# Optimization experiments

Hardware: AMD Instinct MI355X
Metric: run time of the kernel (lower is better)

The kernel has to match this reference:

```python
import jax, jax.numpy as jnp
import numpy as np

B, T, H = 256, 2048, 128
LSTM_IN = [24, 128, 128]


def _xavier(key, fan_out, fan_in):
    std = (2.0 / (fan_in + fan_out)) ** 0.5
    return jax.random.normal(key, (fan_out, fan_in), jnp.float32) * std


def setup_inputs() -> dict:
    key = jax.random.key(0)
    ks = jax.random.split(key, 32)
    inp = {}
    inp['scent'] = jax.random.normal(ks[0], (B, T, 3), jnp.float32)
    # fc1: Linear(3,12) + ReLU + Linear(12,24) + ReLU, xavier weights, zero bias
    inp['W1'] = _xavier(ks[1], 12, 3); inp['b1'] = jnp.zeros((12,), jnp.float32)
    inp['W2'] = _xavier(ks[2], 24, 12); inp['b2'] = jnp.zeros((24,), jnp.float32)
    # 3-layer LSTM, PyTorch default init: uniform(-1/sqrt(H), 1/sqrt(H)) for all params
    k = 1.0 / np.sqrt(H)
    for l in range(3):
        d = LSTM_IN[l]
        inp[f'Wih{l}'] = jax.random.uniform(ks[4 + 4 * l], (4 * H, d), jnp.float32, -k, k)
        inp[f'Whh{l}'] = jax.random.uniform(ks[5 + 4 * l], (4 * H, H), jnp.float32, -k, k)
        inp[f'bih{l}'] = jax.random.uniform(ks[6 + 4 * l], (4 * H,), jnp.float32, -k, k)
        inp[f'bhh{l}'] = jax.random.uniform(ks[7 + 4 * l], (4 * H,), jnp.float32, -k, k)
    # fc2: Linear(128,64) + ReLU + Linear(64,32) + ReLU
    inp['Wf1'] = _xavier(ks[20], 64, 128); inp['bf1'] = jnp.zeros((64,), jnp.float32)
    inp['Wf2'] = _xavier(ks[21], 32, 64); inp['bf2'] = jnp.zeros((32,), jnp.float32)
    return inp


def _lstm_layer(x, Wih, Whh, bih, bhh):
    # x: [T, B, D] -> ys: [T, B, H]; PyTorch gate order i, f, g, o
    gx = jnp.einsum('tbd,gd->tbg', x, Wih) + bih + bhh  # [T, B, 4H]

    def step(carry, g_t):
        h, c = carry
        gates = g_t + h @ Whh.T
        i, f, g, o = jnp.split(gates, 4, axis=-1)
        c = jax.nn.sigmoid(f) * c + jax.nn.sigmoid(i) * jnp.tanh(g)
        h = jax.nn.sigmoid(o) * jnp.tanh(c)
        return (h, c), h

    h0 = jnp.zeros((x.shape[1], H), x.dtype)
    (hT, cT), ys = jax.lax.scan(step, (h0, h0), gx)
    return ys, hT, cT


def reference(scent, W1, b1, W2, b2,
              Wih0, Whh0, bih0, bhh0,
              Wih1, Whh1, bih1, bhh1,
              Wih2, Whh2, bih2, bhh2,
              Wf1, bf1, Wf2, bf2):
    # fc1 (pointwise over B*T)
    x = jax.nn.relu(scent @ W1.T + b1)
    x = jax.nn.relu(x @ W2.T + b2)          # [B, T, 24]
    x = jnp.transpose(x, (1, 0, 2))          # [T, B, 24] seq-first
    hs, cs = [], []
    for Wih, Whh, bih, bhh in ((Wih0, Whh0, bih0, bhh0),
                               (Wih1, Whh1, bih1, bhh1),
                               (Wih2, Whh2, bih2, bhh2)):
        x, hT, cT = _lstm_layer(x, Wih, Whh, bih, bhh)
        hs.append(hT); cs.append(cT)
    h = jnp.stack(hs)                        # [3, B, H]
    c = jnp.stack(cs)                        # [3, B, H]
    y = jnp.transpose(x, (1, 0, 2))          # [B, T, H]
    y = jax.nn.relu(y @ Wf1.T + bf1)
    out = jax.nn.relu(y @ Wf2.T + bf2)       # [B, T, 32]
    return out, h, c
```

## Files before the change

kernel.cpp:

```cpp
#include <hip/hip_runtime.h>

#define B 256
#define T 2048
#define HDIM 128
#define CH 256
#define NCHUNK (T / CH)

typedef _Float16 f16;
typedef _Float16 h2 __attribute__((ext_vector_type(2)));
typedef _Float16 f16x8 __attribute__((ext_vector_type(8)));
typedef float f32x4 __attribute__((ext_vector_type(4)));

__device__ __forceinline__ float dot2(h2 a, h2 b, float c) {
#if __has_builtin(__builtin_amdgcn_fdot2)
    return __builtin_amdgcn_fdot2(a, b, c, false);
#else
    return c + (float)a[0] * (float)b[0] + (float)a[1] * (float)b[1];
#endif
}

__device__ __forceinline__ float rcp_(float x) {
#if __has_builtin(__builtin_amdgcn_rcpf)
    return __builtin_amdgcn_rcpf(x);
#else
    return 1.0f / x;
#endif
}
__device__ __forceinline__ float sigm(float x) { return rcp_(1.0f + __expf(-x)); }
__device__ __forceinline__ float tanh_(float x) {
    float e = __expf(-2.0f * fabsf(x));
    float t = fmaf(2.0f, rcp_(1.0f + e), -1.0f);
    return copysignf(t, x);
}

__device__ __forceinline__ void bar() {
    asm volatile("s_waitcnt lgkmcnt(0)" ::: "memory");
    __builtin_amdgcn_s_barrier();
}

__global__ __launch_bounds__(256) void fc1_kernel(
    const float* __restrict__ scent,
    const float* __restrict__ W1, const float* __restrict__ b1,
    const float* __restrict__ W2, const float* __restrict__ b2,
    f16* __restrict__ x1) {
    int r = blockIdx.x * 256 + threadIdx.x;
    int b = r >> 11, t = r & 2047;
    float s0 = scent[r * 3], s1 = scent[r * 3 + 1], s2 = scent[r * 3 + 2];
    float a[12];
#pragma unroll
    for (int i = 0; i < 12; i++) {
        float v = W1[i * 3] * s0 + W1[i * 3 + 1] * s1 + W1[i * 3 + 2] * s2 + b1[i];
        a[i] = fmaxf(v, 0.f);
    }
    union { f16 o[32]; uint4 u[4]; } U;
#pragma unroll
    for (int j = 0; j < 24; j++) {
        float v = b2[j];
#pragma unroll
        for (int i = 0; i < 12; i++) v = fmaf(W2[j * 12 + i], a[i], v);
        U.o[j] = (f16)fmaxf(v, 0.f);
    }
#pragma unroll
    for (int j = 24; j < 32; j++) U.o[j] = (f16)0.f;
    uint4* d4 = (uint4*)(x1 + ((size_t)t * B + b) * 32);
#pragma unroll
    for (int i = 0; i < 4; i++) d4[i] = U.u[i];
}

__global__ __launch_bounds__(256) void pack_kernel(const float* __restrict__ w,
                                                   unsigned int* __restrict__ o) {
    int i = blockIdx.x * 256 + threadIdx.x;
    if (i < 4096) {
        union { h2 h; unsigned int u; } U;
        U.h[0] = (f16)w[2 * i];
        U.h[1] = (f16)w[2 * i + 1];
        o[i] = U.u;
    }
}

template <int KIN, int KREAL, int SP>
__global__ __launch_bounds__(256) void gx_gemm(
    const f16* __restrict__ x,
    const float* __restrict__ Wih,
    const float* __restrict__ bih, const float* __restrict__ bhh,
    f16* __restrict__ gx,
    int t0) {
    constexpr int KF = KIN / 32;
    __shared__ __align__(16) f16 Alds[64 * SP];
    const int tid = threadIdx.x;
    const int mb = blockIdx.x, nb = blockIdx.y;
    const int l = tid & 63, wv = tid >> 6;
    const int lc = l & 15, lg = l >> 4;

    const f16* xrow = x + ((size_t)t0 * B + (size_t)mb * 64) * KIN;
    if (KIN == 128) {
#pragma unroll
        for (int it = 0; it < 4; it++) {
            int row = it * 16 + (tid >> 4), cc = tid & 15;
            uint4 v = *(const uint4*)(xrow + (size_t)row * KIN + cc * 8);
            *(uint4*)(&Alds[row * SP + cc * 8]) = v;
        }
    } else {
        int row = tid >> 2, cc = tid & 3;
        uint4 v = *(const uint4*)(xrow + (size_t)row * KIN + cc * 8);
        *(uint4*)(&Alds[row * SP + cc * 8]) = v;
    }

    const int gbase = nb * 128 + (wv & 1) * 64;
    const int rbase = (wv >> 1) * 32;
    f16x8 bf[4][KF];
    float bias4[4];
#pragma unroll
    for (int gt = 0; gt < 4; gt++) {
        int g = gbase + gt * 16 + lc;
        bias4[gt] = bih[g] + bhh[g];
#pragma unroll
        for (int kf = 0; kf < KF; kf++) {
            f16x8 v;
#pragma unroll
            for (int j = 0; j < 8; j++) {
                int k = kf * 32 + lg * 8 + j;
                v[j] = (k < KREAL) ? (f16)Wih[(size_t)g * KREAL + k] : (f16)0.f;
            }
            bf[gt][kf] = v;
        }
    }
    __syncthreads();

    f32x4 acc[2][4] = {};
#pragma unroll
    for (int kf = 0; kf < KF; kf++) {
#pragma unroll
        for (int rt = 0; rt < 2; rt++) {
            f16x8 af = *(const f16x8*)(&Alds[(rbase + rt * 16 + lc) * SP + kf * 32 + lg * 8]);
#pragma unroll
            for (int gt = 0; gt < 4; gt++)
                acc[rt][gt] = __builtin_amdgcn_mfma_f32_16x16x32_f16(af, bf[gt][kf], acc[rt][gt], 0, 0, 0);
        }
    }
#pragma unroll
    for (int rt = 0; rt < 2; rt++)
#pragma unroll
        for (int gt = 0; gt < 4; gt++)
#pragma unroll
            for (int q = 0; q < 4; q++) {
                int rr = mb * 64 + rbase + rt * 16 + lg * 4 + q;
                int gg = gbase + gt * 16 + lc;
                gx[(size_t)rr * 512 + gg] = (f16)(acc[rt][gt][q] + bias4[gt]);
            }
}

__global__ __attribute__((amdgpu_flat_work_group_size(512, 512), amdgpu_waves_per_eu(2, 2)))
void lstm_rec(
    const f16* __restrict__ gx,
    const float* __restrict__ Whh,
    f16* __restrict__ y,
    float* __restrict__ hS, float* __restrict__ cS,
    int t0, int init) {
    __shared__ __align__(16) f16 hbuf[2][HDIM];
    const int tid = threadIdx.x, bb = blockIdx.x;
    const int j = tid >> 2, q = tid & 3;

    h2 wh[4][16];
#pragma unroll
    for (int gi = 0; gi < 4; gi++) {
        const float* wr = Whh + (size_t)(gi * 128 + j) * HDIM + 32 * q;
#pragma unroll
        for (int kk = 0; kk < 16; kk++) {
            h2 p; p[0] = (f16)wr[2 * kk]; p[1] = (f16)wr[2 * kk + 1];
            wh[gi][kk] = p;
        }
    }
    float c = 0.f;
    {
        float hv = 0.f;
        if (!init) { hv = hS[bb * HDIM + j]; c = cS[bb * HDIM + j]; }
        if (q == 0) hbuf[0][j] = (f16)hv;
    }
    const ushort* gp = (const ushort*)gx + (size_t)bb * 512 + q * 128 + j;
    ushort gxr[8];
#pragma unroll
    for (int jj = 0; jj < 8; jj++) gxr[jj] = gp[(size_t)jj * (B * 512)];
    __syncthreads();

    float hh = 0.f;
    for (int w8 = 0; w8 < CH / 8; w8++) {
#pragma unroll
        for (int jj = 0; jj < 8; jj++) {
            const int t = w8 * 8 + jj;
            const int p = t & 1;
            union { ushort u; f16 h; } GU; GU.u = gxr[jj];
            float gxv = (float)GU.h;
            int tn = t + 8; if (tn > CH - 1) tn = CH - 1;
            gxr[jj] = gp[(size_t)tn * (B * 512)];

            union { uint4 u[4]; h2 h[16]; } S;
            {
                const uint4* kp = (const uint4*)(&hbuf[p][32 * q]);
                S.u[0] = kp[0]; S.u[1] = kp[1]; S.u[2] = kp[2]; S.u[3] = kp[3];
            }
            float acc[4];
#pragma unroll
            for (int gi = 0; gi < 4; gi++) acc[gi] = (q == gi) ? gxv : 0.f;
#pragma unroll
            for (int kk = 0; kk < 16; kk++) {
#pragma unroll
                for (int gi = 0; gi < 4; gi++) acc[gi] = dot2(wh[gi][kk], S.h[kk], acc[gi]);
            }
#pragma unroll
            for (int gi = 0; gi < 4; gi++) {
                acc[gi] += __shfl_xor(acc[gi], 1);
                acc[gi] += __shfl_xor(acc[gi], 2);
            }
            float gi_ = sigm(acc[0]), gf_ = sigm(acc[1]);
            float gg_ = tanh_(acc[2]), go_ = sigm(acc[3]);
            c = gf_ * c + gi_ * gg_;
            hh = go_ * tanh_(c);
            if (q == 0) {
                hbuf[p ^ 1][j] = (f16)hh;
                y[((size_t)(t0 + t) * B + bb) * HDIM + j] = (f16)hh;
            }
            bar();
        }
    }
    if (q == 0) {
        hS[bb * HDIM + j] = hh;
        cS[bb * HDIM + j] = c;
    }
}

__global__ __launch_bounds__(256) void fc2_kernel(
    const f16* __restrict__ yin,
    const unsigned int* __restrict__ w1,
    const float* __restrict__ bf1,
    const float* __restrict__ Wf2,
    const float* __restrict__ bf2,
    float* __restrict__ out) {
    int r = blockIdx.x * 256 + threadIdx.x;
    union { uint4 u4[16]; h2 h[64]; } Y;
    {
        const uint4* yr4 = (const uint4*)(yin + (size_t)r * 128);
#pragma unroll
        for (int i = 0; i < 16; i++) Y.u4[i] = yr4[i];
    }
    float acc2[32];
#pragma unroll
    for (int i = 0; i < 32; i++) acc2[i] = 0.f;

    for (int cO = 0; cO < 64; cO++) {
        float a0 = bf1[cO], a1 = 0.f, a2 = 0.f, a3 = 0.f;
#pragma unroll
        for (int kk = 0; kk < 64; kk += 4) {
            union { unsigned int u; h2 h; } W0, W1x, W2x, W3;
            W0.u = w1[cO * 64 + kk];      a0 = dot2(W0.h,  Y.h[kk],     a0);
            W1x.u = w1[cO * 64 + kk + 1]; a1 = dot2(W1x.h, Y.h[kk + 1], a1);
            W2x.u = w1[cO * 64 + kk + 2]; a2 = dot2(W2x.h, Y.h[kk + 2], a2);
            W3.u = w1[cO * 64 + kk + 3];  a3 = dot2(W3.h,  Y.h[kk + 3], a3);
        }
        float a = fmaxf((a0 + a1) + (a2 + a3), 0.f);
#pragma unroll
        for (int c2 = 0; c2 < 32; c2++) acc2[c2] = fmaf(a, Wf2[c2 * 64 + cO], acc2[c2]);
    }
    float* orow = out + ((size_t)(r & 255) * T + (r >> 8)) * 32;
#pragma unroll
    for (int c2 = 0; c2 < 32; c2++) orow[c2] = fmaxf(acc2[c2] + bf2[c2], 0.f);
}

extern "C" void kernel_launch(void* const* d_in, const int* in_sizes, int n_in,
                              void* d_out, int out_size, void* d_ws, size_t ws_size,
                              hipStream_t stream) {
    const float* scent = (const float*)d_in[0];
    const float* W1 = (const float*)d_in[1];
    const float* b1 = (const float*)d_in[2];
    const float* W2 = (const float*)d_in[3];
    const float* b2 = (const float*)d_in[4];
    const float* Wih[3] = {(const float*)d_in[5], (const float*)d_in[9], (const float*)d_in[13]};
    const float* Whh[3] = {(const float*)d_in[6], (const float*)d_in[10], (const float*)d_in[14]};
    const float* bihp[3] = {(const float*)d_in[7], (const float*)d_in[11], (const float*)d_in[15]};
    const float* bhhp[3] = {(const float*)d_in[8], (const float*)d_in[12], (const float*)d_in[16]};
    const float* Wf1 = (const float*)d_in[17];
    const float* bf1 = (const float*)d_in[18];
    const float* Wf2 = (const float*)d_in[19];
    const float* bf2 = (const float*)d_in[20];

    const size_t o_x1 = 0;
    const size_t o_y  = 33554432;
    const size_t o_gx = o_y + 134217728;
    const size_t o_w1 = o_gx + 67108864;
    const size_t need = o_w1 + 16384;
    if (ws_size < need) return;

    char* ws = (char*)d_ws;
    f16* x1 = (f16*)(ws + o_x1);
    f16* yb = (f16*)(ws + o_y);
    f16* gxb = (f16*)(ws + o_gx);
    unsigned int* w1p = (unsigned int*)(ws + o_w1);

    float* out = (float*)d_out;
    float* hO = out + (size_t)B * T * 32;
    float* cO = hO + 3 * B * HDIM;

    pack_kernel<<<16, 256, 0, stream>>>(Wf1, w1p);
    fc1_kernel<<<(B * T) / 256, 256, 0, stream>>>(scent, W1, b1, W2, b2, x1);

    dim3 ggrid(CH * B / 64, 4);
    for (int l = 0; l < 3; l++) {
        float* hS = hO + (size_t)l * B * HDIM;
        float* cS = cO + (size_t)l * B * HDIM;
        for (int ch = 0; ch < NCHUNK; ch++) {
            int t0 = ch * CH;
            if (l == 0)
                gx_gemm<32, 24, 40><<<ggrid, 256, 0, stream>>>(x1, Wih[0], bihp[0], bhhp[0], gxb, t0);
            else
                gx_gemm<128, 128, 144><<<ggrid, 256, 0, stream>>>(yb, Wih[l], bihp[l], bhhp[l], gxb, t0);
            lstm_rec<<<B, 512, 0, stream>>>(gxb, Whh[l], yb, hS, cS, t0, ch == 0 ? 1 : 0);
        }
    }
    fc2_kernel<<<(B * T) / 256, 256, 0, stream>>>(yb, w1p, bf1, Wf2, bf2, out);
}
```

Before: 5.664 ms.

## Halve LSTM recurrence threads per hidden unit from four to two

The recurrent kernel now assigns each hidden unit to two threads instead of four, so each block has 256 threads and each thread holds 64 K-elements of all four gate rows (128 h2 registers). Each thread prefetches two gate gx values instead of one, and only a single xor-shuffle reduction is needed. The aim is to shrink the per-step barrier and shuffle cost with fewer waves per block, at the price of twice the dot-product work per thread and heavy register pressure that could cause spills.

```diff
diff --git a/kernel.cpp b/kernel.cpp
--- a/kernel.cpp
+++ b/kernel.cpp
@@ -150,7 +150,7 @@
             }
 }
 
-__global__ __attribute__((amdgpu_flat_work_group_size(512, 512), amdgpu_waves_per_eu(2, 2)))
+__global__ __attribute__((amdgpu_flat_work_group_size(256, 256), amdgpu_waves_per_eu(1, 1)))
 void lstm_rec(
     const f16* __restrict__ gx,
     const float* __restrict__ Whh,
@@ -159,14 +159,14 @@
     int t0, int init) {
     __shared__ __align__(16) f16 hbuf[2][HDIM];
     const int tid = threadIdx.x, bb = blockIdx.x;
-    const int j = tid >> 2, q = tid & 3;
-
-    h2 wh[4][16];
+    const int j = tid >> 1, q = tid & 1;
+
+    h2 wh[4][32];
 #pragma unroll
     for (int gi = 0; gi < 4; gi++) {
-        const float* wr = Whh + (size_t)(gi * 128 + j) * HDIM + 32 * q;
-#pragma unroll
-        for (int kk = 0; kk < 16; kk++) {
+        const float* wr = Whh + (size_t)(gi * 128 + j) * HDIM + 64 * q;
+#pragma unroll
+        for (int kk = 0; kk < 32; kk++) {
             h2 p; p[0] = (f16)wr[2 * kk]; p[1] = (f16)wr[2 * kk + 1];
             wh[gi][kk] = p;
         }
@@ -177,41 +177,48 @@
         if (!init) { hv = hS[bb * HDIM + j]; c = cS[bb * HDIM + j]; }
         if (q == 0) hbuf[0][j] = (f16)hv;
     }
-    const ushort* gp = (const ushort*)gx + (size_t)bb * 512 + q * 128 + j;
-    ushort gxr[8];
-#pragma unroll
-    for (int jj = 0; jj < 8; jj++) gxr[jj] = gp[(size_t)jj * (B * 512)];
+    const ushort* gp0 = (const ushort*)gx + (size_t)bb * 512 + (2 * q) * 128 + j;
+    const ushort* gp1 = gp0 + 128;
+    ushort ga[4], gb[4];
+#pragma unroll
+    for (int jj = 0; jj < 4; jj++) {
+        ga[jj] = gp0[(size_t)jj * (B * 512)];
+        gb[jj] = gp1[(size_t)jj * (B * 512)];
+    }
     __syncthreads();
 
     float hh = 0.f;
-    for (int w8 = 0; w8 < CH / 8; w8++) {
-#pragma unroll
-        for (int jj = 0; jj < 8; jj++) {
-            const int t = w8 * 8 + jj;
+    for (int w4 = 0; w4 < CH / 4; w4++) {
+#pragma unroll
+        for (int jj = 0; jj < 4; jj++) {
+            const int t = w4 * 4 + jj;
             const int p = t & 1;
-            union { ushort u; f16 h; } GU; GU.u = gxr[jj];
-            float gxv = (float)GU.h;
-            int tn = t + 8; if (tn > CH - 1) tn = CH - 1;
-            gxr[jj] = gp[(size_t)tn * (B * 512)];
-
-            union { uint4 u[4]; h2 h[16]; } S;
+            union { ushort u; f16 h; } GA, GB;
+            GA.u = ga[jj]; GB.u = gb[jj];
+            float gxa = (float)GA.h, gxb = (float)GB.h;
+            int tn = t + 4; if (tn > CH - 1) tn = CH - 1;
+            ga[jj] = gp0[(size_t)tn * (B * 512)];
+            gb[jj] = gp1[(size_t)tn * (B * 512)];
+
+            union { uint4 u[8]; h2 h[32]; } S;
             {
-                const uint4* kp = (const uint4*)(&hbuf[p][32 * q]);
-                S.u[0] = kp[0]; S.u[1] = kp[1]; S.u[2] = kp[2]; S.u[3] = kp[3];
+                const uint4* kp = (const uint4*)(&hbuf[p][64 * q]);
+#pragma unroll
+                for (int i = 0; i < 8; i++) S.u[i] = kp[i];
             }
             float acc[4];
-#pragma unroll
-            for (int gi = 0; gi < 4; gi++) acc[gi] = (q == gi) ? gxv : 0.f;
-#pragma unroll
-            for (int kk = 0; kk < 16; kk++) {
+            acc[0] = (q == 0) ? gxa : 0.f;
+            acc[1] = (q == 0) ? gxb : 0.f;
+            acc[2] = (q == 1) ? gxa : 0.f;
+            acc[3] = (q == 1) ? gxb : 0.f;
+#pragma unroll
+            for (int kk = 0; kk < 32; kk++) {
 #pragma unroll
                 for (int gi = 0; gi < 4; gi++) acc[gi] = dot2(wh[gi][kk], S.h[kk], acc[gi]);
             }
 #pragma unroll
-            for (int gi = 0; gi < 4; gi++) {
-                acc[gi] += __shfl_xor(acc[gi], 1);
-                acc[gi] += __shfl_xor(acc[gi], 2);
-            }
+            for (int gi = 0; gi < 4; gi++) acc[gi] += __shfl_xor(acc[gi], 1);
+
             float gi_ = sigm(acc[0]), gf_ = sigm(acc[1]);
             float gg_ = tanh_(acc[2]), go_ = sigm(acc[3]);
             c = gf_ * c + gi_ * gg_;
@@ -313,7 +320,7 @@
                 gx_gemm<32, 24, 40><<<ggrid, 256, 0, stream>>>(x1, Wih[0], bihp[0], bhhp[0], gxb, t0);
             else
                 gx_gemm<128, 128, 144><<<ggrid, 256, 0, stream>>>(yb, Wih[l], bihp[l], bhhp[l], gxb, t0);
-            lstm_rec<<<B, 512, 0, stream>>>(gxb, Whh[l], yb, hS, cS, t0, ch == 0 ? 1 : 0);
+            lstm_rec<<<B, 256, 0, stream>>>(gxb, Whh[l], yb, hS, cS, t0, ch == 0 ? 1 : 0);
         }
     }
     fc2_kernel<<<(B * T) / 256, 256, 0, stream>>>(yb, w1p, bf1, Wf2, bf2, out);
```

Result: faster. 5.214 ms (-7.9%).

## Fuse input-projection GEMM into recurrent LSTM kernel with producer waves

Applied to the files above, without the earlier changes.

Replaces the per-chunk gx_gemm plus lstm_rec launch pairs with one persistent kernel per layer. Four extra waves compute the input projection with MFMA for the next 16 timesteps into double-buffered LDS while eight waves run the recurrence. They also prefetch future input rows from global memory. This removes the gx round trip through global memory and 48 kernel launches, at the cost of a larger block and a 12-wave barrier on every step. It also simplifies tanh by dropping the abs/copysign, and layers 1 and 2 now read and write the same y buffer in place, relying on each block reading future timesteps ahead of its own writes.

```diff
diff --git a/kernel.cpp b/kernel.cpp
--- a/kernel.cpp
+++ b/kernel.cpp
@@ -3,8 +3,6 @@
 #define B 256
 #define T 2048
 #define HDIM 128
-#define CH 256
-#define NCHUNK (T / CH)
 
 typedef _Float16 f16;
 typedef _Float16 h2 __attribute__((ext_vector_type(2)));
@@ -27,10 +25,8 @@
 #endif
 }
 __device__ __forceinline__ float sigm(float x) { return rcp_(1.0f + __expf(-x)); }
-__device__ __forceinline__ float tanh_(float x) {
-    float e = __expf(-2.0f * fabsf(x));
-    float t = fmaf(2.0f, rcp_(1.0f + e), -1.0f);
-    return copysignf(t, x);
+__device__ __forceinline__ float tanh2(float x) {
+    return fmaf(2.0f, rcp_(1.0f + __expf(-2.0f * x)), -1.0f);
 }
 
 __device__ __forceinline__ void bar() {
@@ -78,154 +74,189 @@
     }
 }
 
-template <int KIN, int KREAL, int SP>
-__global__ __launch_bounds__(256) void gx_gemm(
-    const f16* __restrict__ x,
+template <int KF, int KREAL>
+__global__ __attribute__((amdgpu_flat_work_group_size(768, 768), amdgpu_waves_per_eu(3, 3)))
+void lstm_fused(
+    const f16* x,
     const float* __restrict__ Wih,
+    const float* __restrict__ Whh,
     const float* __restrict__ bih, const float* __restrict__ bhh,
-    f16* __restrict__ gx,
-    int t0) {
-    constexpr int KF = KIN / 32;
-    __shared__ __align__(16) f16 Alds[64 * SP];
-    const int tid = threadIdx.x;
-    const int mb = blockIdx.x, nb = blockIdx.y;
-    const int l = tid & 63, wv = tid >> 6;
+    f16* y,
+    float* __restrict__ hT, float* __restrict__ cT) {
+    constexpr int KIN = KF * 32;
+    constexpr int RES = (KF == 1) ? 8 : 4;
+    constexpr int NL = 32 - 4 * RES;
+    __shared__ __align__(16) f16 WiL[(NL > 0 ? NL : 1) * KF * 512];
+    __shared__ __align__(16) f16 xb[2][KF * 512];
+    __shared__ __align__(16) f16 gxw[2][16 * 512];
+    __shared__ __align__(16) f16 hbuf[2][HDIM];
+
+    const int tid = threadIdx.x, bb = blockIdx.x;
+    const int w = tid >> 6, l = tid & 63;
     const int lc = l & 15, lg = l >> 4;
-
-    const f16* xrow = x + ((size_t)t0 * B + (size_t)mb * 64) * KIN;
-    if (KIN == 128) {
-#pragma unroll
-        for (int it = 0; it < 4; it++) {
-            int row = it * 16 + (tid >> 4), cc = tid & 15;
-            uint4 v = *(const uint4*)(xrow + (size_t)row * KIN + cc * 8);
-            *(uint4*)(&Alds[row * SP + cc * 8]) = v;
-        }
+    const int j = (tid & 511) >> 2, q = tid & 3;
+    const int ww = w - 8;
+
+    h2 wh[4][16];
+    float msk[4];
+    float c = 0.f, hl = 0.f;
+    f16x8 resB[RES][KF];
+    float bias8[8];
+    f32x4 acc[8];
+    uint4 xr0;
+
+    if (w < 8) {
+#pragma unroll
+        for (int gi = 0; gi < 4; gi++) {
+            const float* wr = Whh + (size_t)(gi * 128 + j) * HDIM + 32 * q;
+#pragma unroll
+            for (int kk = 0; kk < 16; kk++) {
+                h2 p; p[0] = (f16)wr[2 * kk]; p[1] = (f16)wr[2 * kk + 1];
+                wh[gi][kk] = p;
+            }
+            msk[gi] = (q == gi) ? 1.f : 0.f;
+        }
+        if (q == 0) hbuf[0][j] = (f16)0.f;
     } else {
-        int row = tid >> 2, cc = tid & 3;
-        uint4 v = *(const uint4*)(xrow + (size_t)row * KIN + cc * 8);
-        *(uint4*)(&Alds[row * SP + cc * 8]) = v;
-    }
-
-    const int gbase = nb * 128 + (wv & 1) * 64;
-    const int rbase = (wv >> 1) * 32;
-    f16x8 bf[4][KF];
-    float bias4[4];
-#pragma unroll
-    for (int gt = 0; gt < 4; gt++) {
-        int g = gbase + gt * 16 + lc;
-        bias4[gt] = bih[g] + bhh[g];
-#pragma unroll
-        for (int kf = 0; kf < KF; kf++) {
+#pragma unroll
+        for (int r = 0; r < RES; r++) {
+            int gt = ww * 8 + r;
+#pragma unroll
+            for (int kf = 0; kf < KF; kf++) {
+                f16x8 v;
+#pragma unroll
+                for (int jj = 0; jj < 8; jj++) {
+                    int k = kf * 32 + lg * 8 + jj;
+                    v[jj] = (k < KREAL) ? (f16)Wih[(size_t)(gt * 16 + lc) * KREAL + k] : (f16)0.f;
+                }
+                resB[r][kf] = v;
+            }
+        }
+#pragma unroll
+        for (int gt8 = 0; gt8 < 8; gt8++) {
+            int g = (ww * 8 + gt8) * 16 + lc;
+            bias8[gt8] = bih[g] + bhh[g];
+        }
+    }
+
+    if (NL > 0) {
+        for (int i = tid; i < NL * KF * 64; i += 768) {
+            int gtL = i / (KF * 64);
+            int rem = i - gtL * (KF * 64);
+            int kf = rem >> 6, l2 = rem & 63;
+            int wv2 = gtL / (8 - RES), idx = gtL % (8 - RES);
+            int gt = wv2 * 8 + RES + idx;
+            int g = gt * 16 + (l2 & 15);
             f16x8 v;
 #pragma unroll
-            for (int j = 0; j < 8; j++) {
-                int k = kf * 32 + lg * 8 + j;
-                v[j] = (k < KREAL) ? (f16)Wih[(size_t)g * KREAL + k] : (f16)0.f;
-            }
-            bf[gt][kf] = v;
-        }
+            for (int jj = 0; jj < 8; jj++) {
+                int k = kf * 32 + (l2 >> 4) * 8 + jj;
+                v[jj] = (k < KREAL) ? (f16)Wih[(size_t)g * KREAL + k] : (f16)0.f;
+            }
+            *(f16x8*)(&WiL[(size_t)i * 8]) = v;
+        }
+    }
+    if (w >= 8 && ww < KF) {
+        uint4 a0 = *(const uint4*)(x + (size_t)lc * (B * KIN) + bb * KIN + ww * 32 + lg * 8);
+        uint4 a1 = *(const uint4*)(x + (size_t)(16 + lc) * (B * KIN) + bb * KIN + ww * 32 + lg * 8);
+        *(uint4*)(&xb[0][(ww * 64 + l) * 8]) = a0;
+        *(uint4*)(&xb[1][(ww * 64 + l) * 8]) = a1;
     }
     __syncthreads();
 
-    f32x4 acc[2][4] = {};
-#pragma unroll
-    for (int kf = 0; kf < KF; kf++) {
-#pragma unroll
-        for (int rt = 0; rt < 2; rt++) {
-            f16x8 af = *(const f16x8*)(&Alds[(rbase + rt * 16 + lc) * SP + kf * 32 + lg * 8]);
-#pragma unroll
-            for (int gt = 0; gt < 4; gt++)
-                acc[rt][gt] = __builtin_amdgcn_mfma_f32_16x16x32_f16(af, bf[gt][kf], acc[rt][gt], 0, 0, 0);
-        }
-    }
-#pragma unroll
-    for (int rt = 0; rt < 2; rt++)
-#pragma unroll
-        for (int gt = 0; gt < 4; gt++)
-#pragma unroll
-            for (int q = 0; q < 4; q++) {
-                int rr = mb * 64 + rbase + rt * 16 + lg * 4 + q;
-                int gg = gbase + gt * 16 + lc;
-                gx[(size_t)rr * 512 + gg] = (f16)(acc[rt][gt][q] + bias4[gt]);
-            }
-}
-
-__global__ __attribute__((amdgpu_flat_work_group_size(512, 512), amdgpu_waves_per_eu(2, 2)))
-void lstm_rec(
-    const f16* __restrict__ gx,
-    const float* __restrict__ Whh,
-    f16* __restrict__ y,
-    float* __restrict__ hS, float* __restrict__ cS,
-    int t0, int init) {
-    __shared__ __align__(16) f16 hbuf[2][HDIM];
-    const int tid = threadIdx.x, bb = blockIdx.x;
-    const int j = tid >> 2, q = tid & 3;
-
-    h2 wh[4][16];
-#pragma unroll
-    for (int gi = 0; gi < 4; gi++) {
-        const float* wr = Whh + (size_t)(gi * 128 + j) * HDIM + 32 * q;
-#pragma unroll
-        for (int kk = 0; kk < 16; kk++) {
-            h2 p; p[0] = (f16)wr[2 * kk]; p[1] = (f16)wr[2 * kk + 1];
-            wh[gi][kk] = p;
-        }
-    }
-    float c = 0.f;
-    {
-        float hv = 0.f;
-        if (!init) { hv = hS[bb * HDIM + j]; c = cS[bb * HDIM + j]; }
-        if (q == 0) hbuf[0][j] = (f16)hv;
-    }
-    const ushort* gp = (const ushort*)gx + (size_t)bb * 512 + q * 128 + j;
-    ushort gxr[8];
-#pragma unroll
-    for (int jj = 0; jj < 8; jj++) gxr[jj] = gp[(size_t)jj * (B * 512)];
+    if (w >= 8) {
+        f16x8 af[KF];
+#pragma unroll
+        for (int kf = 0; kf < KF; kf++) af[kf] = *(const f16x8*)(&xb[0][(kf * 64 + l) * 8]);
+#pragma unroll
+        for (int gt8 = 0; gt8 < 8; gt8++) {
+            f32x4 a = {bias8[gt8], bias8[gt8], bias8[gt8], bias8[gt8]};
+#pragma unroll
+            for (int kf = 0; kf < KF; kf++) {
+                f16x8 bf;
+                if (gt8 < RES) bf = resB[gt8 & (RES - 1)][kf];
+                else bf = *(const f16x8*)(&WiL[(size_t)(((ww * (8 - RES) + (gt8 - RES)) * KF + kf) * 64 + l) * 8]);
+                a = __builtin_amdgcn_mfma_f32_16x16x32_f16(af[kf], bf, a, 0, 0, 0);
+            }
+#pragma unroll
+            for (int qq = 0; qq < 4; qq++)
+                gxw[0][(4 * lg + qq) * 512 + (gt8 * 16 + lc) * 4 + ww] = (f16)a[qq];
+        }
+    }
     __syncthreads();
 
-    float hh = 0.f;
-    for (int w8 = 0; w8 < CH / 8; w8++) {
-#pragma unroll
-        for (int jj = 0; jj < 8; jj++) {
-            const int t = w8 * 8 + jj;
-            const int p = t & 1;
-            union { ushort u; f16 h; } GU; GU.u = gxr[jj];
-            float gxv = (float)GU.h;
-            int tn = t + 8; if (tn > CH - 1) tn = CH - 1;
-            gxr[jj] = gp[(size_t)tn * (B * 512)];
-
+    f16* yp = y + (size_t)bb * HDIM + j;
+    for (int t = 0; t < T; t++) {
+        const int s = t & 15, W = t >> 4;
+        const int pg = W & 1, ph = t & 1;
+        if (w < 8) {
+            float gxv = (float)gxw[pg][s * 512 + j * 4 + q];
             union { uint4 u[4]; h2 h[16]; } S;
             {
-                const uint4* kp = (const uint4*)(&hbuf[p][32 * q]);
-                S.u[0] = kp[0]; S.u[1] = kp[1]; S.u[2] = kp[2]; S.u[3] = kp[3];
-            }
-            float acc[4];
-#pragma unroll
-            for (int gi = 0; gi < 4; gi++) acc[gi] = (q == gi) ? gxv : 0.f;
+                const uint4* kp = (const uint4*)(&hbuf[ph][32 * q]);
+#pragma unroll
+                for (int i = 0; i < 4; i++) S.u[i] = kp[i];
+            }
+            float a0 = msk[0] * gxv, a1 = msk[1] * gxv, a2 = msk[2] * gxv, a3 = msk[3] * gxv;
 #pragma unroll
             for (int kk = 0; kk < 16; kk++) {
-#pragma unroll
-                for (int gi = 0; gi < 4; gi++) acc[gi] = dot2(wh[gi][kk], S.h[kk], acc[gi]);
-            }
-#pragma unroll
-            for (int gi = 0; gi < 4; gi++) {
-                acc[gi] += __shfl_xor(acc[gi], 1);
-                acc[gi] += __shfl_xor(acc[gi], 2);
-            }
-            float gi_ = sigm(acc[0]), gf_ = sigm(acc[1]);
-            float gg_ = tanh_(acc[2]), go_ = sigm(acc[3]);
+                a0 = dot2(wh[0][kk], S.h[kk], a0);
+                a1 = dot2(wh[1][kk], S.h[kk], a1);
+                a2 = dot2(wh[2][kk], S.h[kk], a2);
+                a3 = dot2(wh[3][kk], S.h[kk], a3);
+            }
+            a0 += __shfl_xor(a0, 1); a1 += __shfl_xor(a1, 1);
+            a2 += __shfl_xor(a2, 1); a3 += __shfl_xor(a3, 1);
+            a0 += __shfl_xor(a0, 2); a1 += __shfl_xor(a1, 2);
+            a2 += __shfl_xor(a2, 2); a3 += __shfl_xor(a3, 2);
+            float gi_ = sigm(a0), gf_ = sigm(a1), gg_ = tanh2(a2), go_ = sigm(a3);
             c = gf_ * c + gi_ * gg_;
-            hh = go_ * tanh_(c);
+            hl = go_ * tanh2(c);
             if (q == 0) {
-                hbuf[p ^ 1][j] = (f16)hh;
-                y[((size_t)(t0 + t) * B + bb) * HDIM + j] = (f16)hh;
-            }
-            bar();
-        }
-    }
-    if (q == 0) {
-        hS[bb * HDIM + j] = hh;
-        cS[bb * HDIM + j] = c;
+                f16 h16 = (f16)hl;
+                hbuf[ph ^ 1][j] = h16;
+                *yp = h16;
+            }
+            yp += (size_t)B * HDIM;
+        } else {
+            if (s == 1) {
+                f16x8 af[KF];
+#pragma unroll
+                for (int kf = 0; kf < KF; kf++)
+                    af[kf] = *(const f16x8*)(&xb[(W + 1) & 1][(kf * 64 + l) * 8]);
+#pragma unroll
+                for (int gt8 = 0; gt8 < 8; gt8++) {
+                    f32x4 a = {bias8[gt8], bias8[gt8], bias8[gt8], bias8[gt8]};
+#pragma unroll
+                    for (int kf = 0; kf < KF; kf++) {
+                        f16x8 bf;
+                        if (gt8 < RES) bf = resB[gt8 & (RES - 1)][kf];
+                        else bf = *(const f16x8*)(&WiL[(size_t)(((ww * (8 - RES) + (gt8 - RES)) * KF + kf) * 64 + l) * 8]);
+                        a = __builtin_amdgcn_mfma_f32_16x16x32_f16(af[kf], bf, a, 0, 0, 0);
+                    }
+                    acc[gt8] = a;
+                }
+            } else if (s == 3) {
+#pragma unroll
+                for (int gt8 = 0; gt8 < 8; gt8++) {
+#pragma unroll
+                    for (int qq = 0; qq < 4; qq++)
+                        gxw[pg ^ 1][(4 * lg + qq) * 512 + (gt8 * 16 + lc) * 4 + ww] = (f16)acc[gt8][qq];
+                }
+            } else if (s == 6) {
+                if (ww < KF) {
+                    int trow = (W + 2) * 16 + lc; if (trow > T - 1) trow = T - 1;
+                    xr0 = *(const uint4*)(x + (size_t)trow * (B * KIN) + bb * KIN + ww * 32 + lg * 8);
+                }
+            } else if (s == 10) {
+                if (ww < KF) *(uint4*)(&xb[W & 1][(ww * 64 + l) * 8]) = xr0;
+            }
+        }
+        bar();
+    }
+    if (w < 8 && q == 0) {
+        hT[(size_t)bb * HDIM + j] = hl;
+        cT[(size_t)bb * HDIM + j] = c;
     }
 }
 
@@ -285,15 +316,13 @@
 
     const size_t o_x1 = 0;
     const size_t o_y  = 33554432;
-    const size_t o_gx = o_y + 134217728;
-    const size_t o_w1 = o_gx + 67108864;
+    const size_t o_w1 = o_y + 134217728;
     const size_t need = o_w1 + 16384;
     if (ws_size < need) return;
 
     char* ws = (char*)d_ws;
     f16* x1 = (f16*)(ws + o_x1);
     f16* yb = (f16*)(ws + o_y);
-    f16* gxb = (f16*)(ws + o_gx);
     unsigned int* w1p = (unsigned int*)(ws + o_w1);
 
     float* out = (float*)d_out;
@@ -303,18 +332,12 @@
     pack_kernel<<<16, 256, 0, stream>>>(Wf1, w1p);
     fc1_kernel<<<(B * T) / 256, 256, 0, stream>>>(scent, W1, b1, W2, b2, x1);
 
-    dim3 ggrid(CH * B / 64, 4);
-    for (int l = 0; l < 3; l++) {
-        float* hS = hO + (size_t)l * B * HDIM;
-        float* cS = cO + (size_t)l * B * HDIM;
-        for (int ch = 0; ch < NCHUNK; ch++) {
-            int t0 = ch * CH;
-            if (l == 0)
-                gx_gemm<32, 24, 40><<<ggrid, 256, 0, stream>>>(x1, Wih[0], bihp[0], bhhp[0], gxb, t0);
-            else
-                gx_gemm<128, 128, 144><<<ggrid, 256, 0, stream>>>(yb, Wih[l], bihp[l], bhhp[l], gxb, t0);
-            lstm_rec<<<B, 512, 0, stream>>>(gxb, Whh[l], yb, hS, cS, t0, ch == 0 ? 1 : 0);
-        }
-    }
+    lstm_fused<1, 24><<<B, 768, 0, stream>>>(x1, Wih[0], Whh[0], bihp[0], bhhp[0],
+                                             yb, hO, cO);
+    lstm_fused<4, 128><<<B, 768, 0, stream>>>(yb, Wih[1], Whh[1], bihp[1], bhhp[1],
+                                              yb, hO + B * HDIM, cO + B * HDIM);
+    lstm_fused<4, 128><<<B, 768, 0, stream>>>(yb, Wih[2], Whh[2], bihp[2], bhhp[2],
+                                              yb, hO + 2 * B * HDIM, cO + 2 * B * HDIM);
+
     fc2_kernel<<<(B * T) / 256, 256, 0, stream>>>(yb, w1p, bf1, Wf2, bf2, out);
 }
```

New measurement: 5.491 ms. 3.1% less time.
